# Performance work log

Hardware: AMD Instinct MI355X
Metric: run time of the kernel (lower is better)

Reference implementation:

```python
import jax, jax.numpy as jnp
import numpy as np
from jax import lax

EPS = 1e-5
K, S = 7, 4  # patch size / stride, hard-coded in the torch module


def _bn(x, g, b):
    # inference BN with running_mean=0, running_var=1
    return x * (g / np.sqrt(1.0 + EPS)).reshape(1, -1, 1, 1) + b.reshape(1, -1, 1, 1)


def _conv2d(x, w, groups=1, pad=0):
    return lax.conv_general_dilated(
        x, w, (1, 1), [(pad, pad), (pad, pad)],
        dimension_numbers=("NCHW", "OIHW", "NCHW"), feature_group_count=groups)


def _dsconv(x, dw_w, g1, b1, pw_w, g2, b2):
    c_in = x.shape[1]
    y = jax.nn.relu(_bn(_conv2d(x, dw_w, groups=c_in, pad=1), g1, b1))
    y = jax.nn.relu(_bn(_conv2d(y, pw_w, groups=1, pad=0), g2, b2))
    return y


def _unfold(x, nph, npw):
    # torch .unfold(2,K,S).unfold(3,K,S) -> [N,C,nph,npw,K,K]
    idx_h = jnp.arange(nph)[:, None] * S + jnp.arange(K)[None, :]  # [nph,K]
    idx_w = jnp.arange(npw)[:, None] * S + jnp.arange(K)[None, :]  # [npw,K]
    p = x[:, :, idx_h, :]            # [N,C,nph,K,W]
    p = p[:, :, :, :, idx_w]         # [N,C,nph,K,npw,K]
    return p.transpose(0, 1, 2, 4, 3, 5)  # [N,C,nph,npw,K,K]


def setup_inputs() -> dict:
    key = jax.random.key(0)
    ks = jax.random.split(key, 16)
    N, C, H, W = 8, 128, 128, 128
    sc = lambda *s: 1.0 / np.sqrt(np.prod(s[1:])) if len(s) > 1 else 0.02
    d = {
        "exemplar": jax.random.normal(ks[0], (N, C, H, W), jnp.float32),
        "query": jax.random.normal(ks[1], (N, C, H, W), jnp.float32),
        "w_conv_e": jax.random.normal(ks[2], (C, C), jnp.float32) * (1.0 / np.sqrt(C)),
        "w_gate1": jax.random.normal(ks[3], (1, C), jnp.float32) * (1.0 / np.sqrt(C)),
        "w_gate2": jax.random.normal(ks[4], (1, C), jnp.float32) * (1.0 / np.sqrt(C)),
        "dw1_w": jax.random.normal(ks[5], (C, 1, 3, 3), jnp.float32) * (1.0 / 3.0),
        "bn1a_g": jnp.ones((C,), jnp.float32), "bn1a_b": jnp.zeros((C,), jnp.float32),
        "pw1_w": jax.random.normal(ks[6], (C, C, 1, 1), jnp.float32) * (1.0 / np.sqrt(C)),
        "bn1b_g": jnp.ones((C,), jnp.float32), "bn1b_b": jnp.zeros((C,), jnp.float32),
        "dwf_w": jax.random.normal(ks[7], (2 * C, 1, 3, 3), jnp.float32) * (1.0 / 3.0),
        "bnfa_g": jnp.ones((2 * C,), jnp.float32), "bnfa_b": jnp.zeros((2 * C,), jnp.float32),
        "pwf_w": jax.random.normal(ks[8], (C, 2 * C, 1, 1), jnp.float32) * (1.0 / np.sqrt(2 * C)),
        "bnfb_g": jnp.ones((C,), jnp.float32), "bnfb_b": jnp.zeros((C,), jnp.float32),
    }
    return d


def reference(exemplar, query, w_conv_e, w_gate1, w_gate2,
              dw1_w, bn1a_g, bn1a_b, pw1_w, bn1b_g, bn1b_b,
              dwf_w, bnfa_g, bnfa_b, pwf_w, bnfb_g, bnfb_b):
    N, C, H, W = query.shape
    nph = (H - K) // S + 1
    npw = (W - K) // S + 1
    npatch = nph * npw
    D = K * K  # 49

    ex_p = _unfold(exemplar, nph, npw)  # [N,C,nph,npw,K,K]
    q_p = _unfold(query, nph, npw)
    # faithful to torch: raw row-major reinterpretation [N,C,nph,npw,K,K] -> [N*npatch, C, D]
    ex_flat = ex_p.reshape(N * npatch, C, D)
    q_flat = q_p.reshape(N * npatch, C, D)

    ex_corr = jnp.einsum("oc,bcd->bod", w_conv_e, ex_flat)       # conv1d k=1
    A = jnp.einsum("bcd,bce->bde", ex_corr, q_flat)              # [B,D,D]
    A1 = jax.nn.softmax(A, axis=1)
    B2 = jax.nn.softmax(A, axis=2)                               # = softmax(A^T, dim=1) transposed back
    query_att = jnp.einsum("bcd,bde->bce", ex_flat, A1)          # [B,C,D]
    exemplar_att = jnp.einsum("bce,bde->bcd", q_flat, B2)        # [B,C,D]

    def recon(att):
        a = att.reshape(N, nph, npw, C, K, K)
        a = a.transpose(0, 3, 1, 4, 2, 5).reshape(N, C, nph * K, npw * K)
        return a[:, :, :H, :W]

    query_att = recon(query_att)
    exemplar_att = recon(exemplar_att)

    ex_mask = jax.nn.sigmoid(jnp.einsum("oc,nchw->nohw", w_gate1, exemplar_att))
    exemplar_att = exemplar_att * ex_mask
    exemplar_out = _dsconv(exemplar_att + exemplar, dw1_w, bn1a_g, bn1a_b, pw1_w, bn1b_g, bn1b_b)

    q_mask = jax.nn.sigmoid(jnp.einsum("oc,nchw->nohw", w_gate2, query_att))
    query_att = query_att * q_mask
    query_out = _dsconv(query_att + query, dw1_w, bn1a_g, bn1a_b, pw1_w, bn1b_g, bn1b_b)

    pred = _dsconv(jnp.concatenate([exemplar_out, query_out], axis=1),
                   dwf_w, bnfa_g, bnfa_b, pwf_w, bnfb_g, bnfb_b)
    return pred
```

## Files before the change

kernel.cpp:

```cpp
#include <hip/hip_runtime.h>
#include <hip/hip_bf16.h>

#define NN 8
#define CC 128
#define HH 128
#define WW 128
#define HWP (HH*WW)
#define KK 7
#define DD 49
#define NPH 31
#define NPATCH 961
#define PHN 19
#define PAD 52
#define PP2 (PAD*PAD)

typedef __attribute__((ext_vector_type(8))) short bf16x8;
typedef __attribute__((ext_vector_type(4))) float f32x4;
typedef __attribute__((ext_vector_type(4))) unsigned short us4;

__device__ __forceinline__ unsigned short f2bf(float f) {
    unsigned u = __builtin_bit_cast(unsigned, f);
    return (unsigned short)((u + 0x7FFFu + ((u >> 16) & 1u)) >> 16);
}

__global__ __launch_bounds__(512, 4) void attn_kernel(
    const float* __restrict__ ex_g, const float* __restrict__ q_g,
    const float* __restrict__ Wce, const float* __restrict__ wg1,
    const float* __restrict__ wg2,
    float* __restrict__ xe, float* __restrict__ xq)
{
    __shared__ float s_ex[CC*PAD];
    __shared__ float s_q [CC*PAD];
    __shared__ float s_scr[CC*PAD];
    __shared__ float s_m1[PAD], s_l1[PAD], s_m2[PAD], s_l2[PAD];
    __shared__ float s_g1[PAD], s_g2[PAD], s_me[PAD], s_mq[PAD];

    const int t  = threadIdx.x;
    const int n  = blockIdx.y;
    const int ph = blockIdx.x / PHN;
    const int pw = blockIdx.x % PHN;
    const int pp = (ph * NPH + pw) * CC;

    const float* exn = ex_g + (size_t)n * CC * HWP;
    const float* qn  = q_g  + (size_t)n * CC * HWP;

    for (int i = t; i < CC*64; i += 512) {
        int c2 = i >> 6, dl = i & 63;
        if (dl < DD) {
            int kh = dl / KK, kw2 = dl - kh*KK;
            int rem  = pp + c2;
            int c_u  = rem / NPATCH;
            int p_u  = rem - c_u * NPATCH;
            int ph_u = p_u / NPH;
            int pw_u = p_u - ph_u * NPH;
            int gi = (c_u*HH + ph_u*4 + kh)*WW + pw_u*4 + kw2;
            s_ex[c2*PAD + dl] = exn[gi];
            s_q [c2*PAD + dl] = qn [gi];
        }
    }
    if (t < CC*3) {
        int c = t / 3, j = t - (t/3)*3;
        s_ex[c*PAD + DD + j] = 0.f;
        s_q [c*PAD + DD + j] = 0.f;
    }
    __syncthreads();

    {
        const int eg_o = t / 13, eg_d = t - (t/13)*13;
        const int o0 = eg_o*4, d0 = eg_d*4;
        float ac[4][4];
        #pragma unroll
        for (int i = 0; i < 4; ++i)
            #pragma unroll
            for (int j = 0; j < 4; ++j) ac[i][j] = 0.f;
        if (t < 416) {
            for (int k = 0; k < CC; k += 4) {
                float xm[4][4];
                #pragma unroll
                for (int kk = 0; kk < 4; ++kk) {
                    float4 xv = *(const float4*)&s_ex[(k+kk)*PAD + d0];
                    xm[kk][0]=xv.x; xm[kk][1]=xv.y; xm[kk][2]=xv.z; xm[kk][3]=xv.w;
                }
                #pragma unroll
                for (int i = 0; i < 4; ++i) {
                    float4 wv = *(const float4*)&Wce[(o0+i)*CC + k];
                    float wr[4] = {wv.x, wv.y, wv.z, wv.w};
                    #pragma unroll
                    for (int kk = 0; kk < 4; ++kk)
                        #pragma unroll
                        for (int j = 0; j < 4; ++j)
                            ac[i][j] = fmaf(wr[kk], xm[kk][j], ac[i][j]);
                }
            }
        }
        __syncthreads();
        if (t < 416) {
            #pragma unroll
            for (int i = 0; i < 4; ++i)
                *(float4*)&s_scr[(o0+i)*PAD + d0] =
                    make_float4(ac[i][0], ac[i][1], ac[i][2], ac[i][3]);
        }
    }
    __syncthreads();

    float aa[4][2];
    int ad0 = 0, ae0 = 0;
    if (t < 338) {
        int dg = t % 13, eg = t / 13;
        ad0 = dg*4; ae0 = eg*2;
        #pragma unroll
        for (int i = 0; i < 4; ++i) { aa[i][0] = 0.f; aa[i][1] = 0.f; }
        #pragma unroll 4
        for (int k = 0; k < CC; ++k) {
            float4 ev = *(const float4*)&s_scr[k*PAD + ad0];
            float2 qv = *(const float2*)&s_q [k*PAD + ae0];
            #pragma unroll
            for (int i = 0; i < 4; ++i) {
                float e = (i==0)?ev.x:(i==1)?ev.y:(i==2)?ev.z:ev.w;
                aa[i][0] = fmaf(e, qv.x, aa[i][0]);
                aa[i][1] = fmaf(e, qv.y, aa[i][1]);
            }
        }
    } else if (t >= 352 && t < 352 + DD) {
        int e = t - 352;
        float acc = 0.f;
        for (int c = 0; c < CC; ++c) acc = fmaf(wg1[c], s_q[c*PAD + e], acc);
        s_g1[e] = acc;
    } else if (t >= 416 && t < 416 + DD) {
        int d = t - 416;
        float acc = 0.f;
        for (int c = 0; c < CC; ++c) acc = fmaf(wg2[c], s_ex[c*PAD + d], acc);
        s_g2[d] = acc;
    }
    __syncthreads();
    if (t < 338) {
        #pragma unroll
        for (int i = 0; i < 4; ++i)
            *(float2*)&s_scr[(ad0+i)*PAD + ae0] = make_float2(aa[i][0], aa[i][1]);
    }
    __syncthreads();

    if (t < PAD) {
        if (t < DD) {
            float m = -1e30f;
            for (int d = 0; d < DD; ++d) m = fmaxf(m, s_scr[d*PAD + t]);
            float l = 0.f;
            for (int d = 0; d < DD; ++d) l += __expf(s_scr[d*PAD + t] - m);
            s_m1[t] = m; s_l1[t] = 1.f / l;
        } else { s_m1[t] = 0.f; s_l1[t] = 0.f; }
    } else if (t >= 64 && t < 64 + PAD) {
        int d = t - 64;
        if (d < DD) {
            float m = -1e30f;
            for (int e = 0; e < DD; ++e) m = fmaxf(m, s_scr[d*PAD + e]);
            float l = 0.f;
            for (int e = 0; e < DD; ++e) l += __expf(s_scr[d*PAD + e] - m);
            s_m2[d] = m; s_l2[d] = 1.f / l;
        } else { s_m2[d] = 0.f; s_l2[d] = 0.f; }
    }
    __syncthreads();

    float* P1  = s_scr + PP2;
    float* P2T = s_scr;
    {
        float p2buf[6]; int nv = 0;
        for (int i = t; i < PP2; i += 512) {
            int d = i / PAD, e = i - d*PAD;
            float a = s_scr[i];
            P1[i] = __expf(a - s_m1[e]) * s_l1[e];
            p2buf[nv++] = __expf(a - s_m2[d]) * s_l2[d];
        }
        __syncthreads();
        nv = 0;
        for (int i = t; i < PP2; i += 512) {
            int d = i / PAD, e = i - d*PAD;
            P2T[e*PAD + d] = p2buf[nv++];
        }
    }
    __syncthreads();

    if (t < PAD) {
        if (t < DD) {
            float a1 = 0.f, a2 = 0.f;
            for (int e = 0; e < DD; ++e)  a1 = fmaf(s_g1[e],  P2T[e*PAD + t], a1);
            s_me[t] = 1.f / (1.f + __expf(-a1));
            for (int dd = 0; dd < DD; ++dd) a2 = fmaf(s_g2[dd], P1[dd*PAD + t], a2);
            s_mq[t] = 1.f / (1.f + __expf(-a2));
        } else { s_me[t] = 0.f; s_mq[t] = 0.f; }
    }
    __syncthreads();

    float ae[4][4], aq[4][4];
    int c0 = 0, x0 = 0;
    if (t < 416) {
        int cg = t / 13, xg = t - (t/13)*13;
        c0 = cg*4; x0 = xg*4;
        #pragma unroll
        for (int i = 0; i < 4; ++i)
            #pragma unroll
            for (int j = 0; j < 4; ++j) { ae[i][j] = 0.f; aq[i][j] = 0.f; }
        for (int k = 0; k < 48; k += 4) {
            float qm[4][4], xm[4][4], p1m[4][4], p2m[4][4];
            #pragma unroll
            for (int i = 0; i < 4; ++i) {
                float4 qv = *(const float4*)&s_q [(c0+i)*PAD + k];
                float4 xv = *(const float4*)&s_ex[(c0+i)*PAD + k];
                qm[i][0]=qv.x; qm[i][1]=qv.y; qm[i][2]=qv.z; qm[i][3]=qv.w;
                xm[i][0]=xv.x; xm[i][1]=xv.y; xm[i][2]=xv.z; xm[i][3]=xv.w;
            }
            #pragma unroll
            for (int kk = 0; kk < 4; ++kk) {
                float4 p1 = *(const float4*)&P1 [(k+kk)*PAD + x0];
                float4 p2 = *(const float4*)&P2T[(k+kk)*PAD + x0];
                p1m[kk][0]=p1.x; p1m[kk][1]=p1.y; p1m[kk][2]=p1.z; p1m[kk][3]=p1.w;
                p2m[kk][0]=p2.x; p2m[kk][1]=p2.y; p2m[kk][2]=p2.z; p2m[kk][3]=p2.w;
            }
            #pragma unroll
            for (int kk = 0; kk < 4; ++kk)
                #pragma unroll
                for (int i = 0; i < 4; ++i)
                    #pragma unroll
                    for (int j = 0; j < 4; ++j) {
                        ae[i][j] = fmaf(qm[i][kk], p2m[kk][j], ae[i][j]);
                        aq[i][j] = fmaf(xm[i][kk], p1m[kk][j], aq[i][j]);
                    }
        }
        {
            const int k = 48;
            float p1r[4], p2r[4];
            #pragma unroll
            for (int j = 0; j < 4; ++j) { p1r[j] = P1 [k*PAD + x0 + j];
                                          p2r[j] = P2T[k*PAD + x0 + j]; }
            #pragma unroll
            for (int i = 0; i < 4; ++i) {
                float qv = s_q [(c0+i)*PAD + k];
                float xv = s_ex[(c0+i)*PAD + k];
                #pragma unroll
                for (int j = 0; j < 4; ++j) {
                    ae[i][j] = fmaf(qv, p2r[j], ae[i][j]);
                    aq[i][j] = fmaf(xv, p1r[j], aq[i][j]);
                }
            }
        }
    }
    __syncthreads();
    if (t < 416) {
        #pragma unroll
        for (int i = 0; i < 4; ++i) {
            *(float4*)&s_ex[(c0+i)*PAD + x0] =
                make_float4(ae[i][0], ae[i][1], ae[i][2], ae[i][3]);
            *(float4*)&s_q [(c0+i)*PAD + x0] =
                make_float4(aq[i][0], aq[i][1], aq[i][2], aq[i][3]);
        }
    }
    __syncthreads();

    {
        size_t nbase = (size_t)n * CC * HWP;
        int hb = ph*KK, wb = pw*KK;
        for (int i = t; i < CC*DD; i += 512) {
            int c = i / DD, d = i - (i/DD)*DD;
            int kh = d / KK, kw2 = d - kh*KK;
            int h = hb + kh, w = wb + kw2;
            if (h < HH && w < WW) {
                int li = (c*HH + h)*WW + w;
                xe[nbase + li] = s_ex[c*PAD + d] * s_me[d] + exn[li];
                xq[nbase + li] = s_q [c*PAD + d] * s_mq[d] + qn[li];
            }
        }
    }
}

__global__ __launch_bounds__(256) void dw2_kernel(
    const float* __restrict__ xA, unsigned short* __restrict__ yA,
    const float* __restrict__ xB, unsigned short* __restrict__ yB,
    const float* __restrict__ wdw, const float* __restrict__ g,
    const float* __restrict__ b, int CoutTot, int coffA, int coffB)
{
    int bid = blockIdx.x;
    int sel = bid >> 12;
    int idx = (bid & 4095) * 256 + threadIdx.x;
    const float* x = sel ? xB : xA;
    unsigned short* y = sel ? yB : yA;
    int coff          = sel ? coffB : coffA;

    int w4 = (idx & 31) * 4;
    int h4 = ((idx >> 5) & 31) * 4;
    int nc = idx >> 10;
    int c  = nc & 127;
    int n  = nc >> 7;

    const float* wp = wdw + (coff + c) * 9;
    float wr[9];
    #pragma unroll
    for (int i = 0; i < 9; ++i) wr[i] = wp[i];

    const float* base = x + (size_t)nc * HWP;
    float acc[4][4];
    #pragma unroll
    for (int i = 0; i < 4; ++i)
        #pragma unroll
        for (int j = 0; j < 4; ++j) acc[i][j] = 0.f;

    #pragma unroll
    for (int r = 0; r < 6; ++r) {
        int hh = h4 - 1 + r;
        if (hh >= 0 && hh < HH) {
            const float* row = base + hh * WW + w4;
            float4 v = *(const float4*)row;
            float e[6];
            e[0] = (w4 > 0)   ? row[-1] : 0.f;
            e[1] = v.x; e[2] = v.y; e[3] = v.z; e[4] = v.w;
            e[5] = (w4 < 124) ? row[4]  : 0.f;
            int ilo = r - 2 > 0 ? r - 2 : 0;
            int ihi = r < 3 ? r : 3;
            for (int i = ilo; i <= ihi; ++i) {
                int j = r - i;
                float wa = wr[j*3], wb = wr[j*3+1], wc = wr[j*3+2];
                acc[i][0] += wa*e[0] + wb*e[1] + wc*e[2];
                acc[i][1] += wa*e[1] + wb*e[2] + wc*e[3];
                acc[i][2] += wa*e[2] + wb*e[3] + wc*e[4];
                acc[i][3] += wa*e[3] + wb*e[4] + wc*e[5];
            }
        }
    }
    const float rs = 0.99999500003749968f;
    float sc = g[coff + c] * rs, bi = b[coff + c];
    unsigned short* outp = y + (((size_t)n * CoutTot + coff + c) * HH + h4) * WW + w4;
    #pragma unroll
    for (int i = 0; i < 4; ++i) {
        us4 o;
        o[0] = f2bf(fmaxf(acc[i][0] * sc + bi, 0.f));
        o[1] = f2bf(fmaxf(acc[i][1] * sc + bi, 0.f));
        o[2] = f2bf(fmaxf(acc[i][2] * sc + bi, 0.f));
        o[3] = f2bf(fmaxf(acc[i][3] * sc + bi, 0.f));
        *(us4*)(outp + i * WW) = o;
    }
}

#define ZSTR 56

__global__ __launch_bounds__(256, 2) void pw_mfma_kernel(
    const unsigned short* __restrict__ zA, float* __restrict__ outA,
    const unsigned short* __restrict__ zB, float* __restrict__ outB,
    const float* __restrict__ Wp, const float* __restrict__ g,
    const float* __restrict__ b, int Cin)
{
    __shared__ unsigned short s_w[128*ZSTR];
    __shared__ unsigned short s_z[128*ZSTR];

    const int t  = threadIdx.x;
    const int n  = blockIdx.y;
    const int p0 = blockIdx.x * 128;
    const unsigned short* z = blockIdx.z ? zB : zA;
    float* out              = blockIdx.z ? outB : outA;

    const int wave = t >> 6, lane = t & 63;
    const int wo  = (wave & 1) * 64;
    const int wp_ = (wave >> 1) * 64;
    const int lm  = lane & 15, lq = lane >> 4;

    f32x4 acc[4][4];
    #pragma unroll
    for (int i = 0; i < 4; ++i)
        #pragma unroll
        for (int j = 0; j < 4; ++j)
            #pragma unroll
            for (int r = 0; r < 4; ++r) acc[i][j][r] = 0.f;

    const unsigned short* zn = z + (size_t)n * Cin * HWP;

    for (int kb = 0; kb < Cin; kb += 32) {
        {
            int o = t >> 1, cb = (t & 1) * 16;
            const float* wrow = Wp + o * Cin + kb + cb;
            unsigned short* dst = s_w + o * ZSTR + cb;
            #pragma unroll
            for (int i = 0; i < 16; i += 4) {
                float4 v = *(const float4*)(wrow + i);
                dst[i+0] = f2bf(v.x); dst[i+1] = f2bf(v.y);
                dst[i+2] = f2bf(v.z); dst[i+3] = f2bf(v.w);
            }
        }
        {
            int cc = t & 31, pxg = (t >> 5) * 16;
            const unsigned short* src = zn + (size_t)(kb + cc) * HWP + p0 + pxg;
            uint4 a = *(const uint4*)src;
            uint4 b2 = *(const uint4*)(src + 8);
            unsigned v[8] = {a.x, a.y, a.z, a.w, b2.x, b2.y, b2.z, b2.w};
            #pragma unroll
            for (int i = 0; i < 8; ++i) {
                s_z[(pxg + 2*i    ) * ZSTR + cc] = (unsigned short)(v[i] & 0xffffu);
                s_z[(pxg + 2*i + 1) * ZSTR + cc] = (unsigned short)(v[i] >> 16);
            }
        }
        __syncthreads();

        bf16x8 af[4], bfv[4];
        #pragma unroll
        for (int i = 0; i < 4; ++i)
            af[i] = *(const bf16x8*)&s_w[(wo + i*16 + lm) * ZSTR + lq*8];
        #pragma unroll
        for (int j = 0; j < 4; ++j)
            bfv[j] = *(const bf16x8*)&s_z[(wp_ + j*16 + lm) * ZSTR + lq*8];
        #pragma unroll
        for (int i = 0; i < 4; ++i)
            #pragma unroll
            for (int j = 0; j < 4; ++j)
                acc[i][j] = __builtin_amdgcn_mfma_f32_16x16x32_bf16(
                    af[i], bfv[j], acc[i][j], 0, 0, 0);
        __syncthreads();
    }

    const float rs = 0.99999500003749968f;
    float* on = out + (size_t)n * 128 * HWP;
    #pragma unroll
    for (int i = 0; i < 4; ++i) {
        #pragma unroll
        for (int r = 0; r < 4; ++r) {
            int o = wo + i*16 + lq*4 + r;
            float sc = g[o] * rs, bi = b[o];
            #pragma unroll
            for (int j = 0; j < 4; ++j) {
                int px = wp_ + j*16 + lm;
                on[(size_t)o * HWP + p0 + px] =
                    fmaxf(acc[i][j][r] * sc + bi, 0.f);
            }
        }
    }
}

extern "C" void kernel_launch(void* const* d_in, const int* in_sizes, int n_in,
                              void* d_out, int out_size, void* d_ws, size_t ws_size,
                              hipStream_t stream) {
    const float* exemplar = (const float*)d_in[0];
    const float* query    = (const float*)d_in[1];
    const float* w_conv_e = (const float*)d_in[2];
    const float* w_gate1  = (const float*)d_in[3];
    const float* w_gate2  = (const float*)d_in[4];
    const float* dw1_w    = (const float*)d_in[5];
    const float* bn1a_g   = (const float*)d_in[6];
    const float* bn1a_b   = (const float*)d_in[7];
    const float* pw1_w    = (const float*)d_in[8];
    const float* bn1b_g   = (const float*)d_in[9];
    const float* bn1b_b   = (const float*)d_in[10];
    const float* dwf_w    = (const float*)d_in[11];
    const float* bnfa_g   = (const float*)d_in[12];
    const float* bnfa_b   = (const float*)d_in[13];
    const float* pwf_w    = (const float*)d_in[14];
    const float* bnfb_g   = (const float*)d_in[15];
    const float* bnfb_b   = (const float*)d_in[16];

    float* out = (float*)d_out;
    float* ws  = (float*)d_ws;
    const size_t SZ = (size_t)NN * CC * HWP;
    float* bufA = ws;
    float* bufB = ws + SZ;
    unsigned short* zE  = (unsigned short*)(ws + 2*SZ);
    unsigned short* zQ  = zE + SZ;
    unsigned short* T16 = (unsigned short*)(ws + 3*SZ);

    attn_kernel<<<dim3(PHN * PHN, NN), 512, 0, stream>>>(
        exemplar, query, w_conv_e, w_gate1, w_gate2, bufA, bufB);

    dw2_kernel<<<8192, 256, 0, stream>>>(bufA, zE, bufB, zQ,
                                         dw1_w, bn1a_g, bn1a_b, 128, 0, 0);

    pw_mfma_kernel<<<dim3(128, NN, 2), 256, 0, stream>>>(
        zE, bufA, zQ, bufB, pw1_w, bn1b_g, bn1b_b, 128);

    dw2_kernel<<<8192, 256, 0, stream>>>(bufA, T16, bufB, T16,
                                         dwf_w, bnfa_g, bnfa_b, 256, 0, 128);

    pw_mfma_kernel<<<dim3(128, NN, 1), 256, 0, stream>>>(
        T16, out, (const unsigned short*)nullptr, (float*)nullptr,
        pwf_w, bnfb_g, bnfb_b, 256);
}
```

Measured before the change: 682.8 us.

## Overlap query gather with Wce GEMM, vectorize patch loads, parallelize softmax stats

The exemplar patch gather now loads each 7-wide row with float4/float2 loads, and the query patch gather is moved into 64 otherwise idle threads so it runs alongside the Wce projection GEMM, which removes one barrier. The softmax max/sum statistics are split across 4 threads per line with shuffle reductions. The gate-mask sigmoid computation runs on the idle threads during the attention GEMM, which removes another barrier. The write-back is reorganized per row. The float4 loads at pw_u*4 offsets are 16-byte aligned, but the query gather on only 64 threads may become a critical path.

After: 669.3 us. 2.0% less time.

```diff
diff --git a/kernel.cpp b/kernel.cpp
--- a/kernel.cpp
+++ b/kernel.cpp
@@ -44,61 +44,81 @@
     const float* exn = ex_g + (size_t)n * CC * HWP;
     const float* qn  = q_g  + (size_t)n * CC * HWP;
 
-    for (int i = t; i < CC*64; i += 512) {
-        int c2 = i >> 6, dl = i & 63;
-        if (dl < DD) {
-            int kh = dl / KK, kw2 = dl - kh*KK;
-            int rem  = pp + c2;
-            int c_u  = rem / NPATCH;
-            int p_u  = rem - c_u * NPATCH;
-            int ph_u = p_u / NPH;
-            int pw_u = p_u - ph_u * NPH;
-            int gi = (c_u*HH + ph_u*4 + kh)*WW + pw_u*4 + kw2;
-            s_ex[c2*PAD + dl] = exn[gi];
-            s_q [c2*PAD + dl] = qn [gi];
-        }
-    }
-    if (t < CC*3) {
-        int c = t / 3, j = t - (t/3)*3;
-        s_ex[c*PAD + DD + j] = 0.f;
-        s_q [c*PAD + DD + j] = 0.f;
-    }
-    __syncthreads();
-
-    {
-        const int eg_o = t / 13, eg_d = t - (t/13)*13;
+    #pragma unroll
+    for (int ii = 0; ii < 2; ++ii) {
+        const int i  = t + ii*512;
+        const int c2 = i >> 3, kh = i & 7;
+        const int rem  = pp + c2;
+        const int c_u  = rem / NPATCH;
+        const int p_u  = rem - c_u * NPATCH;
+        const int ph_u = p_u / NPH;
+        const int pw_u = p_u - ph_u * NPH;
+        float* de = &s_ex[c2*PAD + kh*KK];
+        if (kh < KK) {
+            const float* se = exn + ((c_u*HH + ph_u*4 + kh)*WW + pw_u*4);
+            const float4 e4 = *(const float4*)se;
+            const float2 e2 = *(const float2*)(se + 4);
+            const float  e1 = se[6];
+            de[0]=e4.x; de[1]=e4.y; de[2]=e4.z; de[3]=e4.w;
+            de[4]=e2.x; de[5]=e2.y; de[6]=e1;
+        } else {
+            de[0]=0.f; de[1]=0.f; de[2]=0.f;
+        }
+    }
+    __syncthreads();
+
+    if (t >= 64 && t < 480) {
+        const int t2 = t - 64;
+        const int eg_o = t2 / 13, eg_d = t2 - (t2/13)*13;
         const int o0 = eg_o*4, d0 = eg_d*4;
         float ac[4][4];
         #pragma unroll
         for (int i = 0; i < 4; ++i)
             #pragma unroll
             for (int j = 0; j < 4; ++j) ac[i][j] = 0.f;
-        if (t < 416) {
-            for (int k = 0; k < CC; k += 4) {
-                float xm[4][4];
-                #pragma unroll
-                for (int kk = 0; kk < 4; ++kk) {
-                    float4 xv = *(const float4*)&s_ex[(k+kk)*PAD + d0];
-                    xm[kk][0]=xv.x; xm[kk][1]=xv.y; xm[kk][2]=xv.z; xm[kk][3]=xv.w;
-                }
-                #pragma unroll
-                for (int i = 0; i < 4; ++i) {
-                    float4 wv = *(const float4*)&Wce[(o0+i)*CC + k];
-                    float wr[4] = {wv.x, wv.y, wv.z, wv.w};
+        for (int k = 0; k < CC; k += 4) {
+            float xm[4][4];
+            #pragma unroll
+            for (int kk = 0; kk < 4; ++kk) {
+                float4 xv = *(const float4*)&s_ex[(k+kk)*PAD + d0];
+                xm[kk][0]=xv.x; xm[kk][1]=xv.y; xm[kk][2]=xv.z; xm[kk][3]=xv.w;
+            }
+            #pragma unroll
+            for (int i = 0; i < 4; ++i) {
+                float4 wv = *(const float4*)&Wce[(o0+i)*CC + k];
+                float wr[4] = {wv.x, wv.y, wv.z, wv.w};
+                #pragma unroll
+                for (int kk = 0; kk < 4; ++kk)
                     #pragma unroll
-                    for (int kk = 0; kk < 4; ++kk)
-                        #pragma unroll
-                        for (int j = 0; j < 4; ++j)
-                            ac[i][j] = fmaf(wr[kk], xm[kk][j], ac[i][j]);
-                }
-            }
-        }
-        __syncthreads();
-        if (t < 416) {
-            #pragma unroll
-            for (int i = 0; i < 4; ++i)
-                *(float4*)&s_scr[(o0+i)*PAD + d0] =
-                    make_float4(ac[i][0], ac[i][1], ac[i][2], ac[i][3]);
+                    for (int j = 0; j < 4; ++j)
+                        ac[i][j] = fmaf(wr[kk], xm[kk][j], ac[i][j]);
+            }
+        }
+        #pragma unroll
+        for (int i = 0; i < 4; ++i)
+            *(float4*)&s_scr[(o0+i)*PAD + d0] =
+                make_float4(ac[i][0], ac[i][1], ac[i][2], ac[i][3]);
+    } else if (t < 64) {
+        #pragma unroll 4
+        for (int jj = 0; jj < 16; ++jj) {
+            const int i  = t + jj*64;
+            const int c2 = i >> 3, kh = i & 7;
+            const int rem  = pp + c2;
+            const int c_u  = rem / NPATCH;
+            const int p_u  = rem - c_u * NPATCH;
+            const int ph_u = p_u / NPH;
+            const int pw_u = p_u - ph_u * NPH;
+            float* dq = &s_q[c2*PAD + kh*KK];
+            if (kh < KK) {
+                const float* sq = qn + ((c_u*HH + ph_u*4 + kh)*WW + pw_u*4);
+                const float4 q4 = *(const float4*)sq;
+                const float2 q2 = *(const float2*)(sq + 4);
+                const float  q1 = sq[6];
+                dq[0]=q4.x; dq[1]=q4.y; dq[2]=q4.z; dq[3]=q4.w;
+                dq[4]=q2.x; dq[5]=q2.y; dq[6]=q1;
+            } else {
+                dq[0]=0.f; dq[1]=0.f; dq[2]=0.f;
+            }
         }
     }
     __syncthreads();
@@ -140,23 +160,50 @@
     }
     __syncthreads();
 
-    if (t < PAD) {
-        if (t < DD) {
-            float m = -1e30f;
-            for (int d = 0; d < DD; ++d) m = fmaxf(m, s_scr[d*PAD + t]);
-            float l = 0.f;
-            for (int d = 0; d < DD; ++d) l += __expf(s_scr[d*PAD + t] - m);
-            s_m1[t] = m; s_l1[t] = 1.f / l;
-        } else { s_m1[t] = 0.f; s_l1[t] = 0.f; }
-    } else if (t >= 64 && t < 64 + PAD) {
-        int d = t - 64;
-        if (d < DD) {
-            float m = -1e30f;
-            for (int e = 0; e < DD; ++e) m = fmaxf(m, s_scr[d*PAD + e]);
-            float l = 0.f;
-            for (int e = 0; e < DD; ++e) l += __expf(s_scr[d*PAD + e] - m);
-            s_m2[d] = m; s_l2[d] = 1.f / l;
-        } else { s_m2[d] = 0.f; s_l2[d] = 0.f; }
+    {
+        const int sub  = t & 3;
+        const int line = (t >> 2) & 63;
+        const int lo   = sub * 13;
+        float v[13];
+        if (t < 256) {
+            if (line < DD) {
+                #pragma unroll
+                for (int j = 0; j < 13; ++j) {
+                    int d = lo + j;
+                    v[j] = (d < DD) ? s_scr[d*PAD + line] : -1e30f;
+                }
+                float m = v[0];
+                #pragma unroll
+                for (int j = 1; j < 13; ++j) m = fmaxf(m, v[j]);
+                m = fmaxf(m, __shfl_xor(m, 1));
+                m = fmaxf(m, __shfl_xor(m, 2));
+                float l = 0.f;
+                #pragma unroll
+                for (int j = 0; j < 13; ++j) l += __expf(v[j] - m);
+                l += __shfl_xor(l, 1);
+                l += __shfl_xor(l, 2);
+                if (sub == 0) { s_m1[line] = m; s_l1[line] = 1.f / l; }
+            } else if (line < PAD && sub == 0) { s_m1[line] = 0.f; s_l1[line] = 0.f; }
+        } else {
+            if (line < DD) {
+                #pragma unroll
+                for (int j = 0; j < 13; ++j) {
+                    int e = lo + j;
+                    v[j] = (e < DD) ? s_scr[line*PAD + e] : -1e30f;
+                }
+                float m = v[0];
+                #pragma unroll
+                for (int j = 1; j < 13; ++j) m = fmaxf(m, v[j]);
+                m = fmaxf(m, __shfl_xor(m, 1));
+                m = fmaxf(m, __shfl_xor(m, 2));
+                float l = 0.f;
+                #pragma unroll
+                for (int j = 0; j < 13; ++j) l += __expf(v[j] - m);
+                l += __shfl_xor(l, 1);
+                l += __shfl_xor(l, 2);
+                if (sub == 0) { s_m2[line] = m; s_l2[line] = 1.f / l; }
+            } else if (line < PAD && sub == 0) { s_m2[line] = 0.f; s_l2[line] = 0.f; }
+        }
     }
     __syncthreads();
 
@@ -179,18 +226,7 @@
     }
     __syncthreads();
 
-    if (t < PAD) {
-        if (t < DD) {
-            float a1 = 0.f, a2 = 0.f;
-            for (int e = 0; e < DD; ++e)  a1 = fmaf(s_g1[e],  P2T[e*PAD + t], a1);
-            s_me[t] = 1.f / (1.f + __expf(-a1));
-            for (int dd = 0; dd < DD; ++dd) a2 = fmaf(s_g2[dd], P1[dd*PAD + t], a2);
-            s_mq[t] = 1.f / (1.f + __expf(-a2));
-        } else { s_me[t] = 0.f; s_mq[t] = 0.f; }
-    }
-    __syncthreads();
-
-    float ae[4][4], aq[4][4];
+    float ae_[4][4], aq_[4][4];
     int c0 = 0, x0 = 0;
     if (t < 416) {
         int cg = t / 13, xg = t - (t/13)*13;
@@ -198,7 +234,7 @@
         #pragma unroll
         for (int i = 0; i < 4; ++i)
             #pragma unroll
-            for (int j = 0; j < 4; ++j) { ae[i][j] = 0.f; aq[i][j] = 0.f; }
+            for (int j = 0; j < 4; ++j) { ae_[i][j] = 0.f; aq_[i][j] = 0.f; }
         for (int k = 0; k < 48; k += 4) {
             float qm[4][4], xm[4][4], p1m[4][4], p2m[4][4];
             #pragma unroll
@@ -221,8 +257,8 @@
                 for (int i = 0; i < 4; ++i)
                     #pragma unroll
                     for (int j = 0; j < 4; ++j) {
-                        ae[i][j] = fmaf(qm[i][kk], p2m[kk][j], ae[i][j]);
-                        aq[i][j] = fmaf(xm[i][kk], p1m[kk][j], aq[i][j]);
+                        ae_[i][j] = fmaf(qm[i][kk], p2m[kk][j], ae_[i][j]);
+                        aq_[i][j] = fmaf(xm[i][kk], p1m[kk][j], aq_[i][j]);
                     }
         }
         {
@@ -237,10 +273,28 @@
                 float xv = s_ex[(c0+i)*PAD + k];
                 #pragma unroll
                 for (int j = 0; j < 4; ++j) {
-                    ae[i][j] = fmaf(qv, p2r[j], ae[i][j]);
-                    aq[i][j] = fmaf(xv, p1r[j], aq[i][j]);
+                    ae_[i][j] = fmaf(qv, p2r[j], ae_[i][j]);
+                    aq_[i][j] = fmaf(xv, p1r[j], aq_[i][j]);
                 }
             }
+        }
+    } else {
+        const int u = t - 416;
+        if (u < DD) {
+            float a1 = 0.f;
+            for (int e = 0; e < DD; ++e) a1 = fmaf(s_g1[e], P2T[e*PAD + u], a1);
+            s_me[u] = 1.f / (1.f + __expf(-a1));
+            if (u < 2) {
+                const int e2 = DD - 2 + u;
+                float a2 = 0.f;
+                for (int d = 0; d < DD; ++d) a2 = fmaf(s_g2[d], P1[d*PAD + e2], a2);
+                s_mq[e2] = 1.f / (1.f + __expf(-a2));
+            }
+        } else {
+            const int e2 = u - DD;
+            float a2 = 0.f;
+            for (int d = 0; d < DD; ++d) a2 = fmaf(s_g2[d], P1[d*PAD + e2], a2);
+            s_mq[e2] = 1.f / (1.f + __expf(-a2));
         }
     }
     __syncthreads();
@@ -248,24 +302,40 @@
         #pragma unroll
         for (int i = 0; i < 4; ++i) {
             *(float4*)&s_ex[(c0+i)*PAD + x0] =
-                make_float4(ae[i][0], ae[i][1], ae[i][2], ae[i][3]);
+                make_float4(ae_[i][0], ae_[i][1], ae_[i][2], ae_[i][3]);
             *(float4*)&s_q [(c0+i)*PAD + x0] =
-                make_float4(aq[i][0], aq[i][1], aq[i][2], aq[i][3]);
+                make_float4(aq_[i][0], aq_[i][1], aq_[i][2], aq_[i][3]);
         }
     }
     __syncthreads();
 
     {
-        size_t nbase = (size_t)n * CC * HWP;
-        int hb = ph*KK, wb = pw*KK;
-        for (int i = t; i < CC*DD; i += 512) {
-            int c = i / DD, d = i - (i/DD)*DD;
-            int kh = d / KK, kw2 = d - kh*KK;
-            int h = hb + kh, w = wb + kw2;
-            if (h < HH && w < WW) {
-                int li = (c*HH + h)*WW + w;
-                xe[nbase + li] = s_ex[c*PAD + d] * s_me[d] + exn[li];
-                xq[nbase + li] = s_q [c*PAD + d] * s_mq[d] + qn[li];
+        const size_t nbase = (size_t)n * CC * HWP;
+        const int hb = ph*KK, wb = pw*KK;
+        const int wlim = (WW - wb) < KK ? (WW - wb) : KK;
+        #pragma unroll
+        for (int ii = 0; ii < 2; ++ii) {
+            const int i  = t + ii*512;
+            const int c  = i >> 3, kh = i & 7;
+            const int h  = hb + kh;
+            if (kh < KK && h < HH) {
+                const int li = (c*HH + h)*WW + wb;
+                const float* sxe = &s_ex[c*PAD + kh*KK];
+                const float* sxq = &s_q [c*PAD + kh*KK];
+                if (wlim == KK) {
+                    #pragma unroll
+                    for (int kw = 0; kw < KK; ++kw) {
+                        const int d = kh*KK + kw;
+                        xe[nbase + li + kw] = sxe[kw]*s_me[d] + exn[li + kw];
+                        xq[nbase + li + kw] = sxq[kw]*s_mq[d] + qn [li + kw];
+                    }
+                } else {
+                    for (int kw = 0; kw < wlim; ++kw) {
+                        const int d = kh*KK + kw;
+                        xe[nbase + li + kw] = sxe[kw]*s_me[d] + exn[li + kw];
+                        xq[nbase + li + kw] = sxq[kw]*s_mq[d] + qn [li + kw];
+                    }
+                }
             }
         }
     }
```
